# Kernel tuning notes

Measured on AMD Instinct MI355X. Metric: run time of the kernel, lower is better.

The kernel has to match this reference:

```python
import jax, jax.numpy as jnp
from jax import lax
import numpy as np

B = 16384

def setup_inputs() -> dict:
    key = jax.random.key(0)
    ks = jax.random.split(key, 48)
    f32 = jnp.float32
    def rn(i, shape, scale=0.05):
        return jax.random.normal(ks[i], shape, dtype=f32) * scale
    d = {}
    d['x'] = jax.random.normal(ks[0], (B, 100), dtype=f32)
    # kaiming-normal initial states: std = sqrt(2/fan_in)
    d['h0f'] = rn(1, (B, 100), np.sqrt(2.0/100))
    d['c0f'] = rn(2, (B, 100), np.sqrt(2.0/100))
    d['h0b'] = rn(3, (B, 100), np.sqrt(2.0/100))
    d['c0b'] = rn(4, (B, 100), np.sqrt(2.0/100))
    d['h0m'] = rn(5, (B, 200), np.sqrt(2.0/200))
    d['c0m'] = rn(6, (B, 200), np.sqrt(2.0/200))
    # LSTMCell(5,100) forward / backward: Wih (400,5), Whh (400,100)
    d['Wih_f'] = rn(7, (400, 5), 0.2); d['Whh_f'] = rn(8, (400, 100), 0.1)
    d['bih_f'] = rn(9, (400,), 0.1);  d['bhh_f'] = rn(10, (400,), 0.1)
    d['Wih_b'] = rn(11, (400, 5), 0.2); d['Whh_b'] = rn(12, (400, 100), 0.1)
    d['bih_b'] = rn(13, (400,), 0.1);  d['bhh_b'] = rn(14, (400,), 0.1)
    # LSTMCell(200,200): Wih (800,200), Whh (800,200)
    d['Wih_m'] = rn(15, (800, 200), 0.07); d['Whh_m'] = rn(16, (800, 200), 0.07)
    d['bih_m'] = rn(17, (800,), 0.07);   d['bhh_m'] = rn(18, (800,), 0.07)
    # dense 200->27
    d['Wd'] = rn(19, (27, 200), 0.07); d['bd'] = rn(20, (27,), 0.07)
    # ConvTranspose1d weights, torch layout (Cin, Cout, K)
    d['w1'] = rn(21, (1, 128, 4), 0.5);  d['b1'] = rn(22, (128,), 0.1)
    d['w2'] = rn(23, (128, 64, 4), 0.04); d['b2'] = rn(24, (64,), 0.1)
    d['w3'] = rn(25, (64, 1, 4), 0.06);  d['b3'] = rn(26, (1,), 0.1)
    # BatchNorm (eval) params/stats
    d['g1'] = jnp.ones((128,), f32); d['be1'] = jnp.zeros((128,), f32)
    d['m1'] = jnp.zeros((128,), f32); d['v1'] = jnp.ones((128,), f32)
    d['g2'] = jnp.ones((64,), f32); d['be2'] = jnp.zeros((64,), f32)
    d['m2'] = jnp.zeros((64,), f32); d['v2'] = jnp.ones((64,), f32)
    return d

def _lstm_step(Wih, Whh, bih, bhh):
    def step(carry, xt):
        h, c = carry
        g = xt @ Wih.T + bih + h @ Whh.T + bhh  # (B, 4H)
        i, f, gg, o = jnp.split(g, 4, axis=1)   # torch gate order i,f,g,o
        c2 = jax.nn.sigmoid(f) * c + jax.nn.sigmoid(i) * jnp.tanh(gg)
        h2 = jax.nn.sigmoid(o) * jnp.tanh(c2)
        return (h2, c2), h2
    return step

def _convT(x, w, b, stride=2, pad=1):
    # torch ConvTranspose1d == conv with lhs_dilation=stride, pad k-1-p, flipped kernel
    k = w.shape[2]
    wc = jnp.transpose(jnp.flip(w, 2), (1, 0, 2))  # (Cout, Cin, K)
    out = lax.conv_general_dilated(x, wc, window_strides=(1,),
                                   padding=[(k - 1 - pad, k - 1 - pad)],
                                   lhs_dilation=(stride,),
                                   dimension_numbers=('NCH', 'OIH', 'NCH'))
    return out + b[None, :, None]

def _bn(x, g, be, m, v, eps=1e-5):
    inv = g / jnp.sqrt(v + eps)
    return (x - m[None, :, None]) * inv[None, :, None] + be[None, :, None]

def reference(x, h0f, c0f, h0b, c0b, h0m, c0m,
              Wih_f, Whh_f, bih_f, bhh_f,
              Wih_b, Whh_b, bih_b, bhh_b,
              Wih_m, Whh_m, bih_m, bhh_m,
              Wd, bd, w1, b1, w2, b2, w3, b3,
              g1, be1, m1, v1, g2, be2, m2, v2):
    xs = x.reshape(20, -1, 5)  # (T=20, B, 5)
    _, hf = lax.scan(_lstm_step(Wih_f, Whh_f, bih_f, bhh_f), (h0f, c0f), xs)
    _, hb = lax.scan(_lstm_step(Wih_b, Whh_b, bih_b, bhh_b), (h0b, c0b), xs, reverse=True)
    merged = jnp.concatenate([hf, hb], axis=-1)  # (20, B, 200)
    (hm, _), _ = lax.scan(_lstm_step(Wih_m, Whh_m, bih_m, bhh_m), (h0m, c0m), merged)
    y = hm @ Wd.T + bd              # dropout in eval mode = identity
    y = y.reshape(-1, 1, 27)
    y = jax.nn.relu(_bn(_convT(y, w1, b1), g1, be1, m1, v1))   # (B,128,54)
    y = jax.nn.relu(_bn(_convT(y, w2, b2), g2, be2, m2, v2))   # (B,64,108)
    y = _convT(y, w3, b3)                                       # (B,1,216)
    return y.reshape(-1, 216)
```

## Files before the change

### kernel.cpp

```cpp
#include <hip/hip_runtime.h>
#include <hip/hip_bf16.h>

#define BTOT 16384

typedef __attribute__((ext_vector_type(8))) short bf16x8;
typedef __attribute__((ext_vector_type(4))) float f32x4;

__device__ __forceinline__ float sig_(float x) {
    return __fdividef(1.0f, 1.0f + __expf(-x));
}
__device__ __forceinline__ float tanh_(float x) {
    float ax = fabsf(x);
    float e  = __expf(-2.0f * ax);
    float r  = __fdividef(1.0f - e, 1.0f + e);
    return x < 0.0f ? -r : r;
}

__global__ __launch_bounds__(256) void k_prep_mfma(
    const float* __restrict__ Wih, const float* __restrict__ Whh,
    const float* __restrict__ bih, const float* __restrict__ bhh,
    __hip_bfloat16* __restrict__ Bhi, __hip_bfloat16* __restrict__ Blo)
{
    const int e = blockIdx.x * 256 + threadIdx.x;
    if (e >= 332800) return;
    const int j  = e & 7;
    const int l  = (e >> 3) & 63;
    const int r2 = e >> 9;
    const int kt = r2 % 13;
    const int ct = r2 / 13;
    const int k  = kt * 32 + ((l >> 4) << 3) + j;
    const int op = ct * 16 + (l & 15);
    const int u  = op >> 2;
    const int g  = op & 3;
    const int row = g * 200 + u;
    float val;
    if (k < 200)       val = Wih[(size_t)row * 200 + k];
    else if (k < 400)  val = Whh[(size_t)row * 200 + (k - 200)];
    else if (k == 415) val = bih[row] + bhh[row];
    else               val = 0.0f;
    const __hip_bfloat16 hi = __float2bfloat16(val);
    Bhi[e] = hi;
    Blo[e] = __float2bfloat16(val - __bfloat162float(hi));
}

__global__ __launch_bounds__(256) void k_prep_mfma100(
    const float* __restrict__ Wih, const float* __restrict__ Whh,
    const float* __restrict__ bih, const float* __restrict__ bhh,
    __hip_bfloat16* __restrict__ Bhi, __hip_bfloat16* __restrict__ Blo)
{
    const int e = blockIdx.x * 256 + threadIdx.x;
    if (e >= 51200) return;
    const int j  = e & 7;
    const int l  = (e >> 3) & 63;
    const int r2 = e >> 9;
    const int kt = r2 & 3;
    const int ct = r2 >> 2;
    const int k  = kt * 32 + ((l >> 4) << 3) + j;
    const int op = ct * 16 + (l & 15);
    const int u  = op >> 2;
    const int g  = op & 3;
    const int row = g * 100 + u;
    float val;
    if (k < 5)         val = Wih[(size_t)row * 5 + k];
    else if (k < 10)   val = Wih[(size_t)row * 5 + (k - 5)];
    else if (k < 110)  val = Whh[(size_t)row * 100 + (k - 10)];
    else if (k == 110) val = bih[row] + bhh[row];
    else               val = 0.0f;
    const __hip_bfloat16 hi = __float2bfloat16(val);
    Bhi[e] = hi;
    Blo[e] = __float2bfloat16(val - __bfloat162float(hi));
}

__global__ __launch_bounds__(512, 2) void k_lstm100(
    const float* __restrict__ x,
    const float* __restrict__ h0f, const float* __restrict__ c0f,
    const float* __restrict__ h0b, const float* __restrict__ c0b,
    const __hip_bfloat16* __restrict__ BFhi, const __hip_bfloat16* __restrict__ BFlo,
    const __hip_bfloat16* __restrict__ BBhi, const __hip_bfloat16* __restrict__ BBlo,
    __hip_bfloat16* __restrict__ HF, __hip_bfloat16* __restrict__ HB)
{
    __shared__ __hip_bfloat16 At[64][136];
    __shared__ float scr[8][16][17];

    const int dir = blockIdx.y;
    const float* h0 = dir ? h0b : h0f;
    const float* c0 = dir ? c0b : c0f;
    const __hip_bfloat16* Bhi = dir ? BBhi : BFhi;
    const __hip_bfloat16* Blo = dir ? BBlo : BFlo;
    __hip_bfloat16* Hout = dir ? HB : HF;

    const int tid = threadIdx.x;
    const int l   = tid & 63;
    const int w   = tid >> 6;
    const int rb  = blockIdx.x * 64;

    float cst[4][4];
    #pragma unroll
    for (int cti = 0; cti < 4; ++cti) {
        const int ct = w + 8 * cti;
        if (ct < 25) {
            #pragma unroll
            for (int rt = 0; rt < 4; ++rt)
                cst[cti][rt] = c0[(size_t)(rb + rt * 16 + (l >> 2)) * 100 + ct * 4 + (l & 3)];
        }
    }

    for (int i = tid; i < 6400; i += 512) {
        const int row = i / 100, u = i - row * 100;
        At[row][10 + u] = __float2bfloat16(h0[(size_t)(rb + row) * 100 + u]);
    }
    for (int i = tid; i < 64 * 26; i += 512) {
        const int row = i / 26, cc = i - row * 26;
        At[row][110 + cc] = __float2bfloat16(cc == 0 ? 1.0f : 0.0f);
    }
    {
        const int tt0 = dir ? 19 : 0;
        if (tid < 320) {
            const float v = x[(size_t)tt0 * (BTOT * 5) + (size_t)rb * 5 + tid];
            const int row = tid / 5, cc = tid - row * 5;
            const __hip_bfloat16 hi = __float2bfloat16(v);
            At[row][cc]     = hi;
            At[row][5 + cc] = __float2bfloat16(v - __bfloat162float(hi));
        }
    }
    __syncthreads();

    for (int t = 0; t < 20; ++t) {
        const int tt = dir ? (19 - t) : t;

        f32x4 acc[4][4];
        #pragma unroll
        for (int cti = 0; cti < 4; ++cti)
            #pragma unroll
            for (int rt = 0; rt < 4; ++rt)
                acc[cti][rt] = (f32x4){0.f, 0.f, 0.f, 0.f};

        #pragma unroll
        for (int kt = 0; kt < 4; ++kt) {
            bf16x8 afr[4];
            #pragma unroll
            for (int rt = 0; rt < 4; ++rt)
                afr[rt] = *reinterpret_cast<const bf16x8*>(
                    &At[rt * 16 + (l & 15)][kt * 32 + (l >> 4) * 8]);
            #pragma unroll
            for (int cti = 0; cti < 4; ++cti) {
                const int ct = w + 8 * cti;
                if (ct < 25) {
                    const size_t fo = ((size_t)(ct * 4 + kt) * 64 + l) * 8;
                    const bf16x8 bh = *reinterpret_cast<const bf16x8*>(Bhi + fo);
                    const bf16x8 bl = *reinterpret_cast<const bf16x8*>(Blo + fo);
                    #pragma unroll
                    for (int rt = 0; rt < 4; ++rt) {
                        acc[cti][rt] = __builtin_amdgcn_mfma_f32_16x16x32_bf16(
                            afr[rt], bh, acc[cti][rt], 0, 0, 0);
                        acc[cti][rt] = __builtin_amdgcn_mfma_f32_16x16x32_bf16(
                            afr[rt], bl, acc[cti][rt], 0, 0, 0);
                    }
                }
            }
        }

        float hval[4][4];
        #pragma unroll
        for (int cti = 0; cti < 4; ++cti) {
            const int ct = w + 8 * cti;
            if (ct < 25) {
                #pragma unroll
                for (int rt = 0; rt < 4; ++rt) {
                    #pragma unroll
                    for (int rr = 0; rr < 4; ++rr)
                        scr[w][(l >> 4) * 4 + rr][l & 15] = acc[cti][rt][rr];
                    const float g0 = scr[w][l >> 2][(l & 3) * 4 + 0];
                    const float g1 = scr[w][l >> 2][(l & 3) * 4 + 1];
                    const float g2 = scr[w][l >> 2][(l & 3) * 4 + 2];
                    const float g3 = scr[w][l >> 2][(l & 3) * 4 + 3];
                    const float ig = sig_(g0);
                    const float fg = sig_(g1);
                    const float gg = tanh_(g2);
                    const float og = sig_(g3);
                    const float cn = fmaf(fg, cst[cti][rt], ig * gg);
                    cst[cti][rt] = cn;
                    hval[cti][rt] = og * tanh_(cn);
                }
            }
        }
        __syncthreads();

        #pragma unroll
        for (int cti = 0; cti < 4; ++cti) {
            const int ct = w + 8 * cti;
            if (ct < 25) {
                #pragma unroll
                for (int rt = 0; rt < 4; ++rt) {
                    const __hip_bfloat16 hb = __float2bfloat16(hval[cti][rt]);
                    At[rt * 16 + (l >> 2)][10 + ct * 4 + (l & 3)] = hb;
                    Hout[((size_t)tt * 100 + ct * 4 + (l & 3)) * BTOT
                         + rb + rt * 16 + (l >> 2)] = hb;
                }
            }
        }
        if (t < 19) {
            const int ttn = dir ? (19 - (t + 1)) : (t + 1);
            if (tid < 320) {
                const float v = x[(size_t)ttn * (BTOT * 5) + (size_t)rb * 5 + tid];
                const int row = tid / 5, cc = tid - row * 5;
                const __hip_bfloat16 hi = __float2bfloat16(v);
                At[row][cc]     = hi;
                At[row][5 + cc] = __float2bfloat16(v - __bfloat162float(hi));
            }
        }
        __syncthreads();
    }
}

__global__ __launch_bounds__(512, 2) void k_mid(
    const float* __restrict__ h0m, const float* __restrict__ c0m,
    const __hip_bfloat16* __restrict__ Bhi, const __hip_bfloat16* __restrict__ Blo,
    const __hip_bfloat16* __restrict__ HF, const __hip_bfloat16* __restrict__ HB,
    __hip_bfloat16* __restrict__ HM)
{
    __shared__ __hip_bfloat16 At[64][424];
    __shared__ float scr[8][16][17];

    const int tid = threadIdx.x;
    const int l   = tid & 63;
    const int w   = tid >> 6;
    const int rb  = blockIdx.x * 64;

    float cst[7][4], hval[7][4];
    #pragma unroll
    for (int cti = 0; cti < 7; ++cti) {
        const int ct = w + 8 * cti;
        if (ct < 50) {
            #pragma unroll
            for (int rt = 0; rt < 4; ++rt) {
                const int row = rb + rt * 16 + (l >> 2);
                cst[cti][rt] = c0m[(size_t)row * 200 + ct * 4 + (l & 3)];
            }
        }
    }

    for (int i = tid; i < 12800; i += 512) {
        const int u = i % 200, rr = i / 200;
        At[rr][200 + u] = __float2bfloat16(h0m[(size_t)(rb + rr) * 200 + u]);
    }
    for (int i = tid; i < 1024; i += 512) {
        const int rr = i >> 4, cc = i & 15;
        At[rr][400 + cc] = __float2bfloat16((cc == 15) ? 1.0f : 0.0f);
    }
    for (int i = tid; i < 6400; i += 512) {
        const int rr = i & 63, u = i >> 6;
        At[rr][u]       = HF[(size_t)u * BTOT + rb + rr];
        At[rr][100 + u] = HB[(size_t)u * BTOT + rb + rr];
    }
    __syncthreads();

    for (int t = 0; t < 20; ++t) {
        #pragma unroll
        for (int cti = 0; cti < 7; ++cti) {
            const int ct = w + 8 * cti;
            if (ct < 50) {
                f32x4 acc[4];
                #pragma unroll
                for (int rt = 0; rt < 4; ++rt) acc[rt] = (f32x4){0.f, 0.f, 0.f, 0.f};
                const __hip_bfloat16* bph = Bhi + ((size_t)ct * 13 * 64 + l) * 8;
                const __hip_bfloat16* bpl = Blo + ((size_t)ct * 13 * 64 + l) * 8;
                const int arow = l & 15;
                const int koff = (l >> 4) * 8;
                #pragma unroll
                for (int kt = 0; kt < 13; ++kt) {
                    const bf16x8 bh = *reinterpret_cast<const bf16x8*>(bph + kt * 512);
                    const bf16x8 bl = *reinterpret_cast<const bf16x8*>(bpl + kt * 512);
                    const int ko = kt * 32 + koff;
                    #pragma unroll
                    for (int rt = 0; rt < 4; ++rt) {
                        const bf16x8 a = *reinterpret_cast<const bf16x8*>(&At[rt * 16 + arow][ko]);
                        acc[rt] = __builtin_amdgcn_mfma_f32_16x16x32_bf16(a, bh, acc[rt], 0, 0, 0);
                        acc[rt] = __builtin_amdgcn_mfma_f32_16x16x32_bf16(a, bl, acc[rt], 0, 0, 0);
                    }
                }
                #pragma unroll
                for (int rt = 0; rt < 4; ++rt) {
                    #pragma unroll
                    for (int rr = 0; rr < 4; ++rr)
                        scr[w][(l >> 4) * 4 + rr][l & 15] = acc[rt][rr];
                    const float g0 = scr[w][l >> 2][(l & 3) * 4 + 0];
                    const float g1 = scr[w][l >> 2][(l & 3) * 4 + 1];
                    const float g2 = scr[w][l >> 2][(l & 3) * 4 + 2];
                    const float g3 = scr[w][l >> 2][(l & 3) * 4 + 3];
                    const float ig = sig_(g0);
                    const float fg = sig_(g1);
                    const float gg = tanh_(g2);
                    const float og = sig_(g3);
                    const float cn = fmaf(fg, cst[cti][rt], ig * gg);
                    cst[cti][rt] = cn;
                    hval[cti][rt] = og * tanh_(cn);
                }
            }
        }
        __syncthreads();

        #pragma unroll
        for (int cti = 0; cti < 7; ++cti) {
            const int ct = w + 8 * cti;
            if (ct < 50) {
                #pragma unroll
                for (int rt = 0; rt < 4; ++rt)
                    At[rt * 16 + (l >> 2)][200 + ct * 4 + (l & 3)] =
                        __float2bfloat16(hval[cti][rt]);
            }
        }
        if (t < 19) {
            const __hip_bfloat16* HFt = HF + (size_t)(t + 1) * 100 * BTOT + rb;
            const __hip_bfloat16* HBt = HB + (size_t)(t + 1) * 100 * BTOT + rb;
            for (int i = tid; i < 6400; i += 512) {
                const int rr = i & 63, u = i >> 6;
                At[rr][u]       = HFt[(size_t)u * BTOT + rr];
                At[rr][100 + u] = HBt[(size_t)u * BTOT + rr];
            }
        }
        __syncthreads();
    }

    for (int i = tid; i < 12800; i += 512) {
        const int u = i % 200, rr = i / 200;
        HM[(size_t)(rb + rr) * 200 + u] = At[rr][200 + u];
    }
}

__global__ __launch_bounds__(256, 2) void k_head(
    const __hip_bfloat16* __restrict__ HM,
    const float* __restrict__ Wd, const float* __restrict__ bd,
    const float* __restrict__ w1, const float* __restrict__ b1,
    const float* __restrict__ w2, const float* __restrict__ b2,
    const float* __restrict__ w3, const float* __restrict__ b3,
    const float* __restrict__ g1, const float* __restrict__ be1,
    const float* __restrict__ m1, const float* __restrict__ v1,
    const float* __restrict__ g2, const float* __restrict__ be2,
    const float* __restrict__ m2, const float* __restrict__ v2,
    float* __restrict__ out)
{
    __shared__ float hm_s[200];
    __shared__ float y27p[29];
    __shared__ float t1p[128][58];
    __shared__ float t2p[64][110];
    __shared__ float sc1[128], sh1[128], sc2[64], sh2[64];

    const int tid = threadIdx.x;
    const int b   = blockIdx.x;

    if (tid < 200) hm_s[tid] = __bfloat162float(HM[(size_t)b * 200 + tid]);
    if (tid < 128) {
        const float s = g1[tid] * __frsqrt_rn(v1[tid] + 1e-5f);
        sc1[tid] = s; sh1[tid] = be1[tid] - m1[tid] * s;
    } else if (tid < 192) {
        const int cc = tid - 128;
        const float s = g2[cc] * __frsqrt_rn(v2[cc] + 1e-5f);
        sc2[cc] = s; sh2[cc] = be2[cc] - m2[cc] * s;
    }
    {
        const int co = tid >> 1;
        t1p[co][(tid & 1) ? 55 : 0] = 0.0f;
        if (tid < 128) { t1p[tid][56] = 0.0f; t1p[tid][57] = 0.0f; }
        if (tid < 64)  { t2p[tid][0] = 0.0f; t2p[tid][109] = 0.0f; }
        if (tid == 0)  { y27p[0] = 0.0f; y27p[28] = 0.0f; }
    }
    __syncthreads();

    if (tid < 27) {
        float a = bd[tid];
        const float* wr = Wd + tid * 200;
        for (int i = 0; i < 200; ++i) a = fmaf(hm_s[i], wr[i], a);
        y27p[tid + 1] = a;
    }
    __syncthreads();

    for (int idx = tid; idx < 128 * 54; idx += 256) {
        const int co = idx / 54;
        const int ll = idx - co * 54;
        const int q  = (ll + 1) >> 1;
        const float4 w = *reinterpret_cast<const float4*>(w1 + co * 4);
        const float wHI = (ll & 1) ? w.x : w.y;
        const float wLO = (ll & 1) ? w.z : w.w;
        float a = b1[co];
        a = fmaf(y27p[q + 1], wHI, a);
        a = fmaf(y27p[q],     wLO, a);
        a = fmaf(a, sc1[co], sh1[co]);
        t1p[co][ll + 1] = fmaxf(a, 0.0f);
    }
    __syncthreads();

    {
        const int co   = tid & 63;
        const int lseg = tid >> 6;
        const int l0   = lseg * 28;
        const int qb   = lseg * 14;
        float acc[28];
        const float bb = b2[co];
        #pragma unroll
        for (int j = 0; j < 28; ++j) acc[j] = bb;

        #pragma unroll 2
        for (int ci = 0; ci < 128; ++ci) {
            float tv[16];
            #pragma unroll
            for (int j = 0; j < 16; ++j) tv[j] = t1p[ci][qb + j];
            const float4 w = *reinterpret_cast<const float4*>(
                w2 + ((size_t)((ci << 6) + co) << 2));
            #pragma unroll
            for (int j = 0; j < 28; ++j) {
                const int qi = (j + 1) >> 1;
                const float wHI = (j & 1) ? w.x : w.y;
                const float wLO = (j & 1) ? w.z : w.w;
                acc[j] = fmaf(tv[qi + 1], wHI, acc[j]);
                acc[j] = fmaf(tv[qi],     wLO, acc[j]);
            }
        }
        const float s2 = sc2[co], h2 = sh2[co];
        #pragma unroll
        for (int j = 0; j < 28; ++j) {
            const int ll = l0 + j;
            if (ll < 108) t2p[co][ll + 1] = fmaxf(fmaf(acc[j], s2, h2), 0.0f);
        }
    }
    __syncthreads();

    if (tid < 216) {
        const int ll = tid;
        const int q = (ll + 1) >> 1;
        const bool odd = (ll & 1) != 0;
        float a = b3[0];
        #pragma unroll 4
        for (int ci = 0; ci < 64; ++ci) {
            const float4 w = *reinterpret_cast<const float4*>(w3 + ci * 4);
            const float wHI = odd ? w.x : w.y;
            const float wLO = odd ? w.z : w.w;
            a = fmaf(t2p[ci][q + 1], wHI, a);
            a = fmaf(t2p[ci][q],     wLO, a);
        }
        out[(size_t)b * 216 + ll] = a;
    }
}

extern "C" void kernel_launch(void* const* d_in, const int* in_sizes, int n_in,
                              void* d_out, int out_size, void* d_ws, size_t ws_size,
                              hipStream_t stream) {
    const float* x     = (const float*)d_in[0];
    const float* h0f   = (const float*)d_in[1];
    const float* c0f   = (const float*)d_in[2];
    const float* h0b   = (const float*)d_in[3];
    const float* c0b   = (const float*)d_in[4];
    const float* h0m   = (const float*)d_in[5];
    const float* c0m   = (const float*)d_in[6];
    const float* Wih_f = (const float*)d_in[7];
    const float* Whh_f = (const float*)d_in[8];
    const float* bih_f = (const float*)d_in[9];
    const float* bhh_f = (const float*)d_in[10];
    const float* Wih_b = (const float*)d_in[11];
    const float* Whh_b = (const float*)d_in[12];
    const float* bih_b = (const float*)d_in[13];
    const float* bhh_b = (const float*)d_in[14];
    const float* Wih_m = (const float*)d_in[15];
    const float* Whh_m = (const float*)d_in[16];
    const float* bih_m = (const float*)d_in[17];
    const float* bhh_m = (const float*)d_in[18];
    const float* Wd    = (const float*)d_in[19];
    const float* bd    = (const float*)d_in[20];
    const float* w1    = (const float*)d_in[21];
    const float* b1    = (const float*)d_in[22];
    const float* w2    = (const float*)d_in[23];
    const float* b2    = (const float*)d_in[24];
    const float* w3    = (const float*)d_in[25];
    const float* b3    = (const float*)d_in[26];
    const float* g1    = (const float*)d_in[27];
    const float* be1   = (const float*)d_in[28];
    const float* m1    = (const float*)d_in[29];
    const float* v1    = (const float*)d_in[30];
    const float* g2    = (const float*)d_in[31];
    const float* be2   = (const float*)d_in[32];
    const float* m2    = (const float*)d_in[33];
    const float* v2    = (const float*)d_in[34];

    char* ws = (char*)d_ws;
    __hip_bfloat16* HF   = (__hip_bfloat16*)ws;
    __hip_bfloat16* HB   = (__hip_bfloat16*)(ws + 65536000);
    __hip_bfloat16* BhiM = (__hip_bfloat16*)(ws + 131072000);
    __hip_bfloat16* BloM = (__hip_bfloat16*)(ws + 131737600);
    __hip_bfloat16* BFhi = (__hip_bfloat16*)(ws + 132403200);
    __hip_bfloat16* BFlo = (__hip_bfloat16*)(ws + 132505600);
    __hip_bfloat16* BBhi = (__hip_bfloat16*)(ws + 132608000);
    __hip_bfloat16* BBlo = (__hip_bfloat16*)(ws + 132710400);
    __hip_bfloat16* HM   = (__hip_bfloat16*)(ws + 132812800);

    k_prep_mfma<<<(332800 + 255) / 256, 256, 0, stream>>>(
        Wih_m, Whh_m, bih_m, bhh_m, BhiM, BloM);
    k_prep_mfma100<<<(51200 + 255) / 256, 256, 0, stream>>>(
        Wih_f, Whh_f, bih_f, bhh_f, BFhi, BFlo);
    k_prep_mfma100<<<(51200 + 255) / 256, 256, 0, stream>>>(
        Wih_b, Whh_b, bih_b, bhh_b, BBhi, BBlo);

    k_lstm100<<<dim3(256, 2), 512, 0, stream>>>(
        x, h0f, c0f, h0b, c0b,
        BFhi, BFlo, BBhi, BBlo, HF, HB);

    k_mid<<<256, 512, 0, stream>>>(
        h0m, c0m, BhiM, BloM, HF, HB, HM);

    k_head<<<16384, 256, 0, stream>>>(
        HM, Wd, bd, w1, b1, w2, b2, w3, b3,
        g1, be1, m1, v1, g2, be2, m2, v2, (float*)d_out);
}
```

Baseline: 2.961 ms.

## Reorder k_mid MFMA loops to reuse A fragments across column tiles with swizzled LDS

```diff
diff --git a/kernel.cpp b/kernel.cpp
--- a/kernel.cpp
+++ b/kernel.cpp
@@ -26,8 +26,8 @@
     const int j  = e & 7;
     const int l  = (e >> 3) & 63;
     const int r2 = e >> 9;
-    const int kt = r2 % 13;
-    const int ct = r2 / 13;
+    const int ct = r2 % 50;
+    const int kt = r2 / 50;
     const int k  = kt * 32 + ((l >> 4) << 3) + j;
     const int op = ct * 16 + (l & 15);
     const int u  = op >> 2;
@@ -213,19 +213,25 @@
     }
 }
 
+__device__ __forceinline__ int aidx(int row, int c) {
+    return (((row >> 4) * 13 + (c >> 5)) * 64 + ((c >> 3) & 3) * 16 + (row & 15)) * 8
+           + (c & 7);
+}
+
 __global__ __launch_bounds__(512, 2) void k_mid(
     const float* __restrict__ h0m, const float* __restrict__ c0m,
     const __hip_bfloat16* __restrict__ Bhi, const __hip_bfloat16* __restrict__ Blo,
     const __hip_bfloat16* __restrict__ HF, const __hip_bfloat16* __restrict__ HB,
     __hip_bfloat16* __restrict__ HM)
 {
-    __shared__ __hip_bfloat16 At[64][424];
+    __shared__ __hip_bfloat16 Af[4][13][64][8];
     __shared__ float scr[8][16][17];
 
     const int tid = threadIdx.x;
     const int l   = tid & 63;
     const int w   = tid >> 6;
     const int rb  = blockIdx.x * 64;
+    __hip_bfloat16* A = &Af[0][0][0][0];
 
     float cst[7][4], hval[7][4];
     #pragma unroll
@@ -242,48 +248,60 @@
 
     for (int i = tid; i < 12800; i += 512) {
         const int u = i % 200, rr = i / 200;
-        At[rr][200 + u] = __float2bfloat16(h0m[(size_t)(rb + rr) * 200 + u]);
+        A[aidx(rr, 200 + u)] = __float2bfloat16(h0m[(size_t)(rb + rr) * 200 + u]);
     }
     for (int i = tid; i < 1024; i += 512) {
         const int rr = i >> 4, cc = i & 15;
-        At[rr][400 + cc] = __float2bfloat16((cc == 15) ? 1.0f : 0.0f);
+        A[aidx(rr, 400 + cc)] = __float2bfloat16((cc == 15) ? 1.0f : 0.0f);
     }
     for (int i = tid; i < 6400; i += 512) {
         const int rr = i & 63, u = i >> 6;
-        At[rr][u]       = HF[(size_t)u * BTOT + rb + rr];
-        At[rr][100 + u] = HB[(size_t)u * BTOT + rb + rr];
+        A[aidx(rr, u)]       = HF[(size_t)u * BTOT + rb + rr];
+        A[aidx(rr, 100 + u)] = HB[(size_t)u * BTOT + rb + rr];
     }
     __syncthreads();
 
     for (int t = 0; t < 20; ++t) {
+        f32x4 acc[7][4];
+        #pragma unroll
+        for (int cti = 0; cti < 7; ++cti)
+            #pragma unroll
+            for (int rt = 0; rt < 4; ++rt)
+                acc[cti][rt] = (f32x4){0.f, 0.f, 0.f, 0.f};
+
+        #pragma unroll
+        for (int kt = 0; kt < 13; ++kt) {
+            bf16x8 afr[4];
+            #pragma unroll
+            for (int rt = 0; rt < 4; ++rt)
+                afr[rt] = *reinterpret_cast<const bf16x8*>(&Af[rt][kt][l][0]);
+            #pragma unroll
+            for (int cti = 0; cti < 7; ++cti) {
+                const int ct = w + 8 * cti;
+                if (ct < 50) {
+                    const size_t fo = ((size_t)(kt * 50 + ct) * 64 + l) * 8;
+                    const bf16x8 bh = *reinterpret_cast<const bf16x8*>(Bhi + fo);
+                    const bf16x8 bl = *reinterpret_cast<const bf16x8*>(Blo + fo);
+                    #pragma unroll
+                    for (int rt = 0; rt < 4; ++rt) {
+                        acc[cti][rt] = __builtin_amdgcn_mfma_f32_16x16x32_bf16(
+                            afr[rt], bh, acc[cti][rt], 0, 0, 0);
+                        acc[cti][rt] = __builtin_amdgcn_mfma_f32_16x16x32_bf16(
+                            afr[rt], bl, acc[cti][rt], 0, 0, 0);
+                    }
+                }
+            }
+        }
+
         #pragma unroll
         for (int cti = 0; cti < 7; ++cti) {
             const int ct = w + 8 * cti;
             if (ct < 50) {
-                f32x4 acc[4];
-                #pragma unroll
-                for (int rt = 0; rt < 4; ++rt) acc[rt] = (f32x4){0.f, 0.f, 0.f, 0.f};
-                const __hip_bfloat16* bph = Bhi + ((size_t)ct * 13 * 64 + l) * 8;
-                const __hip_bfloat16* bpl = Blo + ((size_t)ct * 13 * 64 + l) * 8;
-                const int arow = l & 15;
-                const int koff = (l >> 4) * 8;
-                #pragma unroll
-                for (int kt = 0; kt < 13; ++kt) {
-                    const bf16x8 bh = *reinterpret_cast<const bf16x8*>(bph + kt * 512);
-                    const bf16x8 bl = *reinterpret_cast<const bf16x8*>(bpl + kt * 512);
-                    const int ko = kt * 32 + koff;
-                    #pragma unroll
-                    for (int rt = 0; rt < 4; ++rt) {
-                        const bf16x8 a = *reinterpret_cast<const bf16x8*>(&At[rt * 16 + arow][ko]);
-                        acc[rt] = __builtin_amdgcn_mfma_f32_16x16x32_bf16(a, bh, acc[rt], 0, 0, 0);
-                        acc[rt] = __builtin_amdgcn_mfma_f32_16x16x32_bf16(a, bl, acc[rt], 0, 0, 0);
-                    }
-                }
                 #pragma unroll
                 for (int rt = 0; rt < 4; ++rt) {
                     #pragma unroll
                     for (int rr = 0; rr < 4; ++rr)
-                        scr[w][(l >> 4) * 4 + rr][l & 15] = acc[rt][rr];
+                        scr[w][(l >> 4) * 4 + rr][l & 15] = acc[cti][rt][rr];
                     const float g0 = scr[w][l >> 2][(l & 3) * 4 + 0];
                     const float g1 = scr[w][l >> 2][(l & 3) * 4 + 1];
                     const float g2 = scr[w][l >> 2][(l & 3) * 4 + 2];
@@ -306,7 +324,7 @@
             if (ct < 50) {
                 #pragma unroll
                 for (int rt = 0; rt < 4; ++rt)
-                    At[rt * 16 + (l >> 2)][200 + ct * 4 + (l & 3)] =
+                    A[aidx(rt * 16 + (l >> 2), 200 + ct * 4 + (l & 3))] =
                         __float2bfloat16(hval[cti][rt]);
             }
         }
@@ -315,8 +333,8 @@
             const __hip_bfloat16* HBt = HB + (size_t)(t + 1) * 100 * BTOT + rb;
             for (int i = tid; i < 6400; i += 512) {
                 const int rr = i & 63, u = i >> 6;
-                At[rr][u]       = HFt[(size_t)u * BTOT + rr];
-                At[rr][100 + u] = HBt[(size_t)u * BTOT + rr];
+                A[aidx(rr, u)]       = HFt[(size_t)u * BTOT + rr];
+                A[aidx(rr, 100 + u)] = HBt[(size_t)u * BTOT + rr];
             }
         }
         __syncthreads();
@@ -324,7 +342,7 @@
 
     for (int i = tid; i < 12800; i += 512) {
         const int u = i % 200, rr = i / 200;
-        HM[(size_t)(rb + rr) * 200 + u] = At[rr][200 + u];
+        HM[(size_t)(rb + rr) * 200 + u] = A[aidx(rr, 200 + u)];
     }
 }
 
```

New measurement: 3.418 ms. 1.15x slower.
